# Optimization experiments

Hardware: AMD Instinct MI355X
Metric: run time of the kernel (lower is better)

Reference implementation:

```python
import jax, jax.numpy as jnp
import numpy as np

N_HEAD = 16
EPS = 1e-06


def setup_inputs() -> dict:
    key = jax.random.key(0)
    ks = jax.random.split(key, 9)
    B, S, Q, D, Dp = 16, 4096, 49, 1024, 1024
    INIT = 0.02  # GPT-2 style init scale keeps exp(scores) finite
    x = jax.random.normal(ks[0], (B, S, D), dtype=jnp.float32)
    y = jax.random.normal(ks[1], (B, Q, Dp), dtype=jnp.float32)
    # multiplicative binary mask applied to exp(scores), shaped [1,1,49,S//64,64]
    attention_mask = (jax.random.uniform(ks[2], (1, 1, Q, S // 64, 64)) > 0.5).astype(jnp.float32)
    W_attn = jax.random.normal(ks[3], (D, 2 * D), dtype=jnp.float32) * INIT
    b_attn = jnp.zeros((2 * D,), dtype=jnp.float32)
    W_mlp = jax.random.normal(ks[4], (Dp, D), dtype=jnp.float32) * INIT
    b_mlp = jnp.zeros((D,), dtype=jnp.float32)
    W_proj = jax.random.normal(ks[5], (D, Dp), dtype=jnp.float32) * INIT
    b_proj = jnp.zeros((Dp,), dtype=jnp.float32)
    return {"x": x, "y": y, "attention_mask": attention_mask,
            "W_attn": W_attn, "b_attn": b_attn, "W_mlp": W_mlp, "b_mlp": b_mlp,
            "W_proj": W_proj, "b_proj": b_proj}


def reference(x, y, attention_mask, W_attn, b_attn, W_mlp, b_mlp, W_proj, b_proj):
    B, S, D = x.shape
    Q = y.shape[1]
    H = N_HEAD
    hd = D // H
    # c_attn (Conv1D): x @ W + b -> split into key, value
    kv = x @ W_attn + b_attn                       # [B,S,2D]
    key, value = kv[..., :D], kv[..., D:]
    k = key.reshape(B, S, H, hd).transpose(0, 2, 3, 1)    # [B,H,hd,S] (k=True perm)
    v = value.reshape(B, S, H, hd).transpose(0, 2, 1, 3)  # [B,H,S,hd]
    q = (y @ W_mlp + b_mlp).reshape(B, Q, H, hd).transpose(0, 2, 1, 3)  # [B,H,Q,hd]
    # fp32 scores, scaled by sqrt(head_dim)
    w = jnp.einsum('bhqd,bhds->bhqs', q.astype(jnp.float32), k.astype(jnp.float32))
    w = w / jnp.sqrt(jnp.float32(hd))
    # custom exp + multiplicative blocked mask + epsilon-stabilized normalize
    e = (jnp.exp(w).reshape(B, H, 49, -1, 64) * attention_mask).reshape(B, H, Q, S)
    w = e / (e.sum(-1, keepdims=True) + EPS)
    # PV matmul, cast to bf16 as in the original, then merge heads
    a = jnp.einsum('bhqs,bhsd->bhqd', w, v.astype(jnp.float32)).astype(jnp.bfloat16)
    a = a.transpose(0, 2, 1, 3).reshape(B, Q, D).astype(jnp.float32)
    out = a @ W_proj + b_proj                      # c_proj
    return out
```

## Files before the change

### kernel.cpp

```cpp
#include <hip/hip_runtime.h>
#include <cstdint>

typedef __bf16 bf16x8 __attribute__((ext_vector_type(8)));
typedef float f32x4 __attribute__((ext_vector_type(4)));
typedef unsigned short u16;

#define GBAR() asm volatile("s_barrier" ::: "memory")
#define SBAR0() __builtin_amdgcn_sched_barrier(0)
#define LGKM0() do { asm volatile("s_waitcnt lgkmcnt(0)" ::: "memory"); SBAR0(); } while (0)
#define VM6()  asm volatile("s_waitcnt vmcnt(6)" ::: "memory")
#define VM8()  asm volatile("s_waitcnt vmcnt(8)" ::: "memory")
#define MFMA16(a, b, c) __builtin_amdgcn_mfma_f32_16x16x32_bf16((a), (b), (c), 0, 0, 0)

__device__ __forceinline__ u16 f2bf(float f) {
  unsigned u = __builtin_bit_cast(unsigned, f);
  u += 0x7fffu + ((u >> 16) & 1u);
  return (u16)(u >> 16);
}
__device__ __forceinline__ float bfu(ushort4 v, int r) {
  unsigned short s = (r == 0) ? v.x : (r == 1) ? v.y : (r == 2) ? v.z : v.w;
  return __builtin_bit_cast(float, (unsigned)s << 16);
}

__global__ void cast_f32_bf16(const float* __restrict__ in, u16* __restrict__ out,
                              int n4in, int n4out) {
  int i = blockIdx.x * blockDim.x + threadIdx.x;
  int stride = gridDim.x * blockDim.x;
  for (; i < n4out; i += stride) {
    ushort4 o;
    if (i < n4in) {
      float4 v = ((const float4*)in)[i];
      o.x = f2bf(v.x); o.y = f2bf(v.y); o.z = f2bf(v.z); o.w = f2bf(v.w);
    } else {
      o.x = 0; o.y = 0; o.z = 0; o.w = 0;
    }
    ((ushort4*)out)[i] = o;
  }
}

__global__ void transpose_cast(const float* __restrict__ in, u16* __restrict__ out,
                               int R, int C) {
  __shared__ float t[64][65];
  int tc = blockIdx.x * 64, tr = blockIdx.y * 64;
  int c = threadIdx.x & 63, r0 = threadIdx.x >> 6;
  #pragma unroll
  for (int p = 0; p < 16; ++p) {
    int r = p * 4 + r0;
    t[r][c] = in[(long)(tr + r) * C + (tc + c)];
  }
  __syncthreads();
  #pragma unroll
  for (int p = 0; p < 16; ++p) {
    int r = p * 4 + r0;
    out[(long)(tc + r) * R + (tr + c)] = f2bf(t[c][r]);
  }
}

__global__ void mask_prep(const float* __restrict__ in, u16* __restrict__ out) {
  __shared__ float t[64][65];
  int s0 = blockIdx.x * 64;
  int c = threadIdx.x & 63, r0 = threadIdx.x >> 6;
  #pragma unroll
  for (int p = 0; p < 16; ++p) {
    int q = p * 4 + r0;
    t[q][c] = (q < 49) ? in[(long)q * 4096 + s0 + c] : 0.f;
  }
  __syncthreads();
  #pragma unroll
  for (int p = 0; p < 16; ++p) {
    int r = p * 4 + r0;
    out[(long)(s0 + r) * 64 + c] = f2bf(t[c][r]);
  }
}

template<int MODE>
__global__ __launch_bounds__(512, 2) void gemm256(
    const u16* __restrict__ A, const u16* __restrict__ BT,
    const float* __restrict__ bias, void* __restrict__ outp)
{
  __shared__ __align__(16) char lds[131072];

  int tid = threadIdx.x;
  int l = tid & 63, w = tid >> 6;
  int wr = w >> 2, wc = w & 3;
  int lr = l & 15, lh = l >> 4;

  int bid = blockIdx.x;
  int mt, nt;
  long out_off = 0;
  const u16* Ap = A;
  const u16* BTp = BT;
  if constexpr (MODE == 0) {
    int wg = (bid & 7) * 128 + (bid >> 3);
    mt = wg >> 2; nt = wg & 3;
  } else {
    int wg = (bid & 7) * 8 + (bid >> 3);
    mt = wg & 3; nt = wg >> 2;
    int b = blockIdx.y;
    BTp = BT + (long)b * 4194304;
    out_off = (long)b * 4194304;
  }
  long Arow0 = (long)mt * 256;
  long Brow0 = (long)nt * 256;

  int rho = (w << 3) + (l >> 3);
  int csw = ((l & 7) ^ (l >> 3)) << 3;
  const u16* agA = Ap + (Arow0 + rho) * 1024 + csw;
  int browoff = (w >> 2) * 64 + (w & 3) * 8 + (l >> 3);
  const u16* agB = BTp + (Brow0 + browoff) * 1024 + csw;
  char* ldsAthr = lds + rho * 128 + (l & 7) * 16;
  char* ldsBthr = lds + 32768 + browoff * 128 + (l & 7) * 16;

  auto SA = [&](int dt, int st, int mh) {
    char* d = ldsAthr + (dt & 1) * 65536 + mh * 8192;
    const u16* s = agA + (long)st * 64 + mh * 65536;
    __builtin_amdgcn_global_load_lds(
        (const __attribute__((address_space(1))) void*)s,
        (__attribute__((address_space(3))) void*)d, 16, 0, 0);
    __builtin_amdgcn_global_load_lds(
        (const __attribute__((address_space(1))) void*)(s + 131072),
        (__attribute__((address_space(3))) void*)(d + 16384), 16, 0, 0);
  };
  auto SB = [&](int dt, int st, int h) {
    char* d = ldsBthr + (dt & 1) * 65536 + h * 4096;
    const u16* s = agB + (long)st * 64 + h * 32768;
    __builtin_amdgcn_global_load_lds(
        (const __attribute__((address_space(1))) void*)s,
        (__attribute__((address_space(3))) void*)d, 16, 0, 0);
    __builtin_amdgcn_global_load_lds(
        (const __attribute__((address_space(1))) void*)(s + 131072),
        (__attribute__((address_space(3))) void*)(d + 16384), 16, 0, 0);
  };

  int arow_b = (wr * 128 + lr) * 128;
  int brow_b = (wc * 64 + lr) * 128 + 32768;
  int xr0 = (lh ^ (lr & 7)) << 4;
  int xr1 = ((4 + lh) ^ (lr & 7)) << 4;

  f32x4 acc[8][4];
  #pragma unroll
  for (int m = 0; m < 8; ++m)
    #pragma unroll
    for (int n = 0; n < 4; ++n) acc[m][n] = f32x4{0.f, 0.f, 0.f, 0.f};

  bf16x8 af[4][2], bn0[2][2], bn1[2][2];

  auto RD_AF0 = [&](int buf) {
    #pragma unroll
    for (int m = 0; m < 4; ++m) {
      af[m][0] = *(const bf16x8*)(lds + buf + arow_b + m * 2048 + xr0);
      af[m][1] = *(const bf16x8*)(lds + buf + arow_b + m * 2048 + xr1);
    }
  };
  auto RD_AF1 = [&](int buf) {
    #pragma unroll
    for (int m = 0; m < 4; ++m) {
      af[m][0] = *(const bf16x8*)(lds + buf + arow_b + 8192 + m * 2048 + xr0);
      af[m][1] = *(const bf16x8*)(lds + buf + arow_b + 8192 + m * 2048 + xr1);
    }
  };
  auto RD_BN0 = [&](int buf) {
    #pragma unroll
    for (int n = 0; n < 2; ++n) {
      bn0[n][0] = *(const bf16x8*)(lds + buf + brow_b + n * 2048 + xr0);
      bn0[n][1] = *(const bf16x8*)(lds + buf + brow_b + n * 2048 + xr1);
    }
  };
  auto RD_BN1 = [&](int buf) {
    #pragma unroll
    for (int n = 0; n < 2; ++n) {
      bn1[n][0] = *(const bf16x8*)(lds + buf + brow_b + 4096 + n * 2048 + xr0);
      bn1[n][1] = *(const bf16x8*)(lds + buf + brow_b + 4096 + n * 2048 + xr1);
    }
  };
  auto Q = [&](int mo, int no, bf16x8 (&bn)[2][2]) {
    __builtin_amdgcn_s_setprio(1);
    #pragma unroll
    for (int m = 0; m < 4; ++m)
      #pragma unroll
      for (int n = 0; n < 2; ++n) {
        acc[mo + m][no + n] = MFMA16(af[m][0], bn[n][0], acc[mo + m][no + n]);
        acc[mo + m][no + n] = MFMA16(af[m][1], bn[n][1], acc[mo + m][no + n]);
      }
    __builtin_amdgcn_s_setprio(0);
  };

  SA(0, 0, 0); SA(0, 0, 1); SB(0, 0, 0); SB(0, 0, 1);
  SA(1, 1, 0); SA(1, 1, 1); SB(1, 1, 0);
  VM6(); GBAR();

  for (int i = 0; i < 8; ++i) {
    int t = 2 * i;
    RD_AF0(0); RD_BN0(0); SBAR0();
    SB(t + 1, t + 1, 1);
    GBAR(); LGKM0();
    Q(0, 0, bn0);
    GBAR();
    RD_BN1(0); SBAR0();
    { int tt = t + 2; SA(tt, tt < 16 ? tt : 15, 0); }
    GBAR(); LGKM0();
    Q(0, 2, bn1);
    GBAR();
    RD_AF1(0); SBAR0();
    { int tt = t + 2; SB(tt, tt < 16 ? tt : 15, 0); }
    GBAR(); LGKM0();
    Q(4, 0, bn0);
    GBAR();
    { int tt = t + 2; SA(tt, tt < 16 ? tt : 15, 1); }
    GBAR(); VM6();
    Q(4, 2, bn1);
    GBAR();
    RD_AF0(65536); RD_BN0(65536); SBAR0();
    { int tt = t + 2; SB(tt, tt < 16 ? tt : 15, 1); }
    GBAR(); LGKM0();
    Q(0, 0, bn0);
    GBAR();
    RD_BN1(65536); SBAR0();
    { int tt = t + 3; SA(tt, tt < 16 ? tt : 15, 0); }
    GBAR(); LGKM0();
    Q(0, 2, bn1);
    GBAR();
    RD_AF1(65536); SBAR0();
    { int tt = t + 3; SB(tt, tt < 16 ? tt : 15, 0); }
    GBAR(); LGKM0();
    Q(4, 0, bn0);
    GBAR();
    { int tt = t + 3; SA(tt, tt < 16 ? tt : 15, 1); }
    GBAR(); VM6();
    Q(4, 2, bn1);
    GBAR();
  }

  asm volatile("s_waitcnt vmcnt(0)" ::: "memory");

  #pragma unroll
  for (int m = 0; m < 8; ++m) {
    #pragma unroll
    for (int n = 0; n < 4; ++n) {
      #pragma unroll
      for (int r = 0; r < 4; ++r) {
        long row = Arow0 + wr * 128 + m * 16 + lh * 4 + r;
        long col = Brow0 + wc * 64 + n * 16 + lr;
        float v = acc[m][n][r];
        if constexpr (MODE == 0) {
          v += bias[col];
          long addr = (row >> 12) * 4194304 + (col >> 6) * 262144
                    + (row & 4095) * 64 + (col & 63);
          ((u16*)outp)[addr] = f2bf(v);
        } else {
          v += bias[1024 + row];
          ((u16*)outp)[out_off + row * 4096 + col] = f2bf(v);
        }
      }
    }
  }
}

template<int MODE>
__global__ __launch_bounds__(256, 2) void gemm_bt(
    const u16* __restrict__ A, const u16* __restrict__ BT,
    const float* __restrict__ bias, void* __restrict__ outp)
{
  __shared__ u16 As[128][64];
  __shared__ u16 Bs[128][64];

  int bid = blockIdx.x;
  int mt = bid >> 3, nt = bid & 7;

  int tid = threadIdx.x;
  int l = tid & 63, w = tid >> 6;
  int wr = w >> 1, wc = w & 1;
  int lr = l & 15, lh = l >> 4;

  f32x4 acc[4][4];
  #pragma unroll
  for (int i = 0; i < 4; ++i)
    #pragma unroll
    for (int j = 0; j < 4; ++j)
      acc[i][j] = f32x4{0.f, 0.f, 0.f, 0.f};

  long arow0 = (long)mt * 128;
  long brow0 = (long)nt * 128;
  int srow = w * 8 + (l >> 3);
  int scol = (l & 7) * 8;
  const u16* ag = A + (arow0 + srow) * 1024 + scol;
  const u16* bg = BT + (brow0 + srow) * 1024 + scol;
  u16* asl = &As[srow][scol];
  u16* bsl = &Bs[srow][scol];

  for (int kt = 0; kt < 16; ++kt) {
    int ko = kt * 64;
    #pragma unroll
    for (int p = 0; p < 4; ++p)
      __builtin_amdgcn_global_load_lds(
          (const __attribute__((address_space(1))) void*)(ag + (long)p * 32 * 1024 + ko),
          (__attribute__((address_space(3))) void*)(asl + p * 32 * 64), 16, 0, 0);
    #pragma unroll
    for (int p = 0; p < 4; ++p)
      __builtin_amdgcn_global_load_lds(
          (const __attribute__((address_space(1))) void*)(bg + (long)p * 32 * 1024 + ko),
          (__attribute__((address_space(3))) void*)(bsl + p * 32 * 64), 16, 0, 0);
    __syncthreads();
    #pragma unroll
    for (int kk = 0; kk < 2; ++kk) {
      bf16x8 af[4], bfr[4];
      #pragma unroll
      for (int m = 0; m < 4; ++m)
        af[m] = *(const bf16x8*)&As[wr * 64 + m * 16 + lr][kk * 32 + lh * 8];
      #pragma unroll
      for (int n = 0; n < 4; ++n)
        bfr[n] = *(const bf16x8*)&Bs[wc * 64 + n * 16 + lr][kk * 32 + lh * 8];
      #pragma unroll
      for (int m = 0; m < 4; ++m)
        #pragma unroll
        for (int n = 0; n < 4; ++n)
          acc[m][n] = MFMA16(af[m], bfr[n], acc[m][n]);
    }
    __syncthreads();
  }

  #pragma unroll
  for (int m = 0; m < 4; ++m) {
    #pragma unroll
    for (int n = 0; n < 4; ++n) {
      #pragma unroll
      for (int r = 0; r < 4; ++r) {
        int row = (int)arow0 + wr * 64 + m * 16 + lh * 4 + r;
        int col = (int)brow0 + wc * 64 + n * 16 + lr;
        float v = acc[m][n][r];
        if constexpr (MODE == 2) {
          if (row < 784) {
            v += bias[col];
            int b = row / 49, qi = row - b * 49;
            long addr = ((long)(b * 16 + (col >> 6)) * 64 + qi) * 64 + (col & 63);
            ((u16*)outp)[addr] = f2bf(v);
          }
        } else {
          if (row < 784) {
            v += bias[col];
            ((float*)outp)[(long)row * 1024 + col] = v;
          }
        }
      }
    }
  }
}

__global__ __launch_bounds__(256, 4) void attn_part(
    const u16* __restrict__ Kt, const u16* __restrict__ Vt, const u16* __restrict__ Q,
    const u16* __restrict__ maskT,
    float* __restrict__ partA, float* __restrict__ prs)
{
  __shared__ __align__(16) char lds[40960];

  int bh = blockIdx.x, chunk = blockIdx.y;
  int tid = threadIdx.x;
  int l = tid & 63, w = tid >> 6;
  int lr = l & 15, lh = l >> 4;

  const u16* Kb = Kt + (long)bh * 262144;
  const u16* Vb = Vt + (long)bh * 262144;
  const u16* Qb = Q + (long)bh * 4096;

  int t0 = chunk * 21 + (chunk > 0 ? 1 : 0);
  int nt = 21 + (chunk == 0 ? 1 : 0);
  int tmax = t0 + nt - 1;

  int strow = tid >> 3;
  int sc = tid & 7;

  auto STAGE = [&](int buf, int tt) {
    long s0 = (long)tt * 64;
    #pragma unroll
    for (int h = 0; h < 2; ++h) {
      int row = h * 32 + strow;
      int cs = (sc ^ (row & 7)) << 3;
      const u16* ksrc = Kb + (s0 + row) * 64 + cs;
      char* kdst = lds + buf * 8192 + row * 128 + sc * 16;
      __builtin_amdgcn_global_load_lds(
          (const __attribute__((address_space(1))) void*)ksrc,
          (__attribute__((address_space(3))) void*)kdst, 16, 0, 0);
      const u16* vsrc = Vb + (long)row * 4096 + s0 + cs;
      char* vdst = lds + 16384 + buf * 8192 + row * 128 + sc * 16;
      __builtin_amdgcn_global_load_lds(
          (const __attribute__((address_space(1))) void*)vsrc,
          (__attribute__((address_space(3))) void*)vdst, 16, 0, 0);
    }
  };

  bf16x8 qf[2];
  #pragma unroll
  for (int kf2 = 0; kf2 < 2; ++kf2)
    qf[kf2] = *(const bf16x8*)(Qb + (w * 16 + lr) * 64 + kf2 * 32 + lh * 8);

  bf16x8 ones;
  #pragma unroll
  for (int j = 0; j < 8; ++j) ones[j] = (__bf16)1.0f;

  f32x4 acc_a[4];
  #pragma unroll
  for (int n = 0; n < 4; ++n) acc_a[n] = f32x4{0.f, 0.f, 0.f, 0.f};
  f32x4 acc_rs = f32x4{0.f, 0.f, 0.f, 0.f};

  char* Pw = lds + 32768 + w * 2048;
  const u16* mbase = maskT + w * 16 + lh * 4;

  STAGE(0, t0);
  STAGE(1, t0 + 1);
  ushort4 mvu[4];
  #pragma unroll
  for (int sf = 0; sf < 4; ++sf)
    mvu[sf] = *(const ushort4*)(mbase + ((long)t0 * 64 + sf * 16 + lr) * 64);
  VM8();
  GBAR();

  for (int it = 0; it < nt; ++it) {
    int buf = it & 1;
    const char* Kl = lds + buf * 8192;
    const char* Vl = lds + 16384 + buf * 8192;

    int tn = it + 1 < nt ? t0 + it + 1 : tmax;
    ushort4 mvn[4];
    #pragma unroll
    for (int sf = 0; sf < 4; ++sf)
      mvn[sf] = *(const ushort4*)(mbase + ((long)tn * 64 + sf * 16 + lr) * 64);

    bf16x8 kf[4][2];
    #pragma unroll
    for (int sf = 0; sf < 4; ++sf) {
      int srw = sf * 16 + lr;
      int xb = srw & 7;
      kf[sf][0] = *(const bf16x8*)(Kl + srw * 128 + ((lh ^ xb) << 4));
      kf[sf][1] = *(const bf16x8*)(Kl + srw * 128 + (((4 + lh) ^ xb) << 4));
    }
    f32x4 lg[4];
    #pragma unroll
    for (int sf = 0; sf < 4; ++sf) {
      f32x4 t = f32x4{0.f, 0.f, 0.f, 0.f};
      t = MFMA16(qf[0], kf[sf][0], t);
      t = MFMA16(qf[1], kf[sf][1], t);
      lg[sf] = t;
    }

    bf16x8 vf[2][4];
    #pragma unroll
    for (int k2 = 0; k2 < 2; ++k2)
      #pragma unroll
      for (int n = 0; n < 4; ++n) {
        int vrow = n * 16 + lr;
        vf[k2][n] = *(const bf16x8*)(Vl + vrow * 128 + (((k2 * 4 + lh) ^ (lr & 7)) << 4));
      }

    #pragma unroll
    for (int sf = 0; sf < 4; ++sf) {
      #pragma unroll
      for (int r = 0; r < 4; ++r) {
        int qq = lh * 4 + r;
        float e = __expf(lg[sf][r] * 0.125f) * bfu(mvu[sf], r);
        int byte = (qq * 128 + (sf * 16 + lr) * 2) ^ ((qq & 7) << 4);
        *(u16*)(Pw + byte) = f2bf(e);
      }
    }

    #pragma unroll
    for (int k2 = 0; k2 < 2; ++k2) {
      int byte = (lr * 128 + k2 * 64 + lh * 16) ^ ((lr & 7) << 4);
      bf16x8 pf;
      __builtin_memcpy(&pf, Pw + byte, 16);
      #pragma unroll
      for (int n = 0; n < 4; ++n)
        acc_a[n] = MFMA16(pf, vf[k2][n], acc_a[n]);
      acc_rs = MFMA16(pf, ones, acc_rs);
    }

    LGKM0();
    GBAR();
    { int tt = it + 2 < nt ? t0 + it + 2 : tmax; STAGE(buf, tt); }
    VM8();
    GBAR();

    #pragma unroll
    for (int sf = 0; sf < 4; ++sf) mvu[sf] = mvn[sf];
  }

  long base = ((long)bh * 3 + chunk) * 64;
  #pragma unroll
  for (int r = 0; r < 4; ++r) {
    int q = w * 16 + lh * 4 + r;
    if (lr == 0) prs[base + q] = acc_rs[r];
    #pragma unroll
    for (int n = 0; n < 4; ++n)
      partA[(base + q) * 64 + n * 16 + lr] = acc_a[n][r];
  }
}

__global__ __launch_bounds__(256) void attn_reduce(
    const float* __restrict__ partA, const float* __restrict__ prs,
    u16* __restrict__ Abf)
{
  int bh = blockIdx.x;
  int t = threadIdx.x;
  int q = t >> 2, d0 = (t & 3) * 16;
  if (q >= 49) return;
  int b = bh >> 4, h = bh & 15;

  float rs = 1e-6f;
  #pragma unroll
  for (int c = 0; c < 3; ++c) rs += prs[((long)bh * 3 + c) * 64 + q];

  #pragma unroll
  for (int j = 0; j < 4; ++j) {
    float4 s = float4{0.f, 0.f, 0.f, 0.f};
    #pragma unroll
    for (int c = 0; c < 3; ++c) {
      float4 v = *(const float4*)(partA + (((long)bh * 3 + c) * 64 + q) * 64 + d0 + j * 4);
      s.x += v.x; s.y += v.y; s.z += v.z; s.w += v.w;
    }
    ushort4 o;
    o.x = f2bf(s.x / rs); o.y = f2bf(s.y / rs);
    o.z = f2bf(s.z / rs); o.w = f2bf(s.w / rs);
    *(ushort4*)(Abf + ((long)(b * 49 + q) * 1024 + h * 64 + d0 + j * 4)) = o;
  }
}

extern "C" void kernel_launch(void* const* d_in, const int* in_sizes, int n_in,
                              void* d_out, int out_size, void* d_ws, size_t ws_size,
                              hipStream_t stream) {
  const float* x      = (const float*)d_in[0];
  const float* y      = (const float*)d_in[1];
  const float* mask   = (const float*)d_in[2];
  const float* W_attn = (const float*)d_in[3];
  const float* b_attn = (const float*)d_in[4];
  const float* W_mlp  = (const float*)d_in[5];
  const float* b_mlp  = (const float*)d_in[6];
  const float* W_proj = (const float*)d_in[7];
  const float* b_proj = (const float*)d_in[8];

  if (ws_size < 417333248ULL) return;

  char* ws = (char*)d_ws;
  u16* x_bf    = (u16*)(ws);
  u16* Kt      = (u16*)(ws + 134217728L);
  u16* Vt      = (u16*)(ws + 268435456L);
  u16* WT_attn = (u16*)(ws + 402653184L);
  u16* WT_mlp  = (u16*)(ws + 406847488L);
  u16* WT_proj = (u16*)(ws + 408944640L);
  u16* y_bf    = (u16*)(ws + 411041792L);
  u16* q_ws    = (u16*)(ws + 412876800L);
  u16* a_bf    = (u16*)(ws + 414973952L);
  u16* maskT   = (u16*)(ws + 416808960L);
  float* partA = (float*)(ws);
  float* prs   = (float*)(ws + 16777216L);

  cast_f32_bf16<<<2048, 256, 0, stream>>>(x, x_bf, 16777216, 16777216);
  cast_f32_bf16<<<896, 256, 0, stream>>>(y, y_bf, 200704, 229376);
  transpose_cast<<<dim3(32, 16), 256, 0, stream>>>(W_attn, WT_attn, 1024, 2048);
  transpose_cast<<<dim3(16, 16), 256, 0, stream>>>(W_mlp, WT_mlp, 1024, 1024);
  transpose_cast<<<dim3(16, 16), 256, 0, stream>>>(W_proj, WT_proj, 1024, 1024);
  mask_prep<<<64, 256, 0, stream>>>(mask, maskT);

  gemm256<0><<<1024, 512, 0, stream>>>(x_bf, WT_attn, b_attn, Kt);
  gemm256<1><<<dim3(64, 16), 512, 0, stream>>>(WT_attn + 1048576, x_bf, b_attn, Vt);
  gemm_bt<2><<<56, 256, 0, stream>>>(y_bf, WT_mlp, b_mlp, q_ws);

  attn_part<<<dim3(256, 3), 256, 0, stream>>>(Kt, Vt, q_ws, maskT, partA, prs);
  attn_reduce<<<256, 256, 0, stream>>>(partA, prs, a_bf);

  gemm_bt<3><<<56, 256, 0, stream>>>(a_bf, WT_proj, b_proj, d_out);
}
```

Measured before the change: 493.0 us.

## Retile small GEMMs to 64x64, fuse y cast, merge transposes, split attention into 4 chunks

Replaces the 128x128 small-GEMM kernel with a 64x64 tile version using an XOR-swizzled LDS layout. The Q projection now reads fp32 y directly and converts it to bf16 while staging, which removes the separate y cast kernel. The three weight transpose launches become one launch with a z dimension, and attention is split into 4 equal chunks of 16 tiles instead of 3 uneven ones. The goal is more blocks for the small GEMMs and attention on many CUs and fewer launches, at the cost of more partial sums to reduce.

```diff
diff --git a/kernel.cpp b/kernel.cpp
--- a/kernel.cpp
+++ b/kernel.cpp
@@ -23,24 +23,28 @@
 }
 
 __global__ void cast_f32_bf16(const float* __restrict__ in, u16* __restrict__ out,
-                              int n4in, int n4out) {
+                              int n4) {
   int i = blockIdx.x * blockDim.x + threadIdx.x;
   int stride = gridDim.x * blockDim.x;
-  for (; i < n4out; i += stride) {
+  for (; i < n4; i += stride) {
+    float4 v = ((const float4*)in)[i];
     ushort4 o;
-    if (i < n4in) {
-      float4 v = ((const float4*)in)[i];
-      o.x = f2bf(v.x); o.y = f2bf(v.y); o.z = f2bf(v.z); o.w = f2bf(v.w);
-    } else {
-      o.x = 0; o.y = 0; o.z = 0; o.w = 0;
-    }
+    o.x = f2bf(v.x); o.y = f2bf(v.y); o.z = f2bf(v.z); o.w = f2bf(v.w);
     ((ushort4*)out)[i] = o;
   }
 }
 
-__global__ void transpose_cast(const float* __restrict__ in, u16* __restrict__ out,
-                               int R, int C) {
+__global__ void transpose_all(const float* __restrict__ Wa, const float* __restrict__ Wm,
+                              const float* __restrict__ Wp,
+                              u16* __restrict__ oa, u16* __restrict__ om,
+                              u16* __restrict__ op) {
   __shared__ float t[64][65];
+  int z = blockIdx.z;
+  const float* in = (z == 0) ? Wa : (z == 1) ? Wm : Wp;
+  u16* out = (z == 0) ? oa : (z == 1) ? om : op;
+  int C = (z == 0) ? 2048 : 1024;
+  const int R = 1024;
+  if (blockIdx.x * 64 >= C) return;
   int tc = blockIdx.x * 64, tr = blockIdx.y * 64;
   int c = threadIdx.x & 63, r0 = threadIdx.x >> 6;
   #pragma unroll
@@ -257,87 +261,99 @@
 }
 
 template<int MODE>
-__global__ __launch_bounds__(256, 2) void gemm_bt(
-    const u16* __restrict__ A, const u16* __restrict__ BT,
+__global__ __launch_bounds__(256, 4) void gemm64(
+    const void* __restrict__ Ap, const u16* __restrict__ BT,
     const float* __restrict__ bias, void* __restrict__ outp)
 {
-  __shared__ u16 As[128][64];
-  __shared__ u16 Bs[128][64];
+  __shared__ u16 As[64][64];
+  __shared__ u16 Bs[64][64];
 
   int bid = blockIdx.x;
-  int mt = bid >> 3, nt = bid & 7;
-
+  int mt = bid >> 4, nt = bid & 15;
   int tid = threadIdx.x;
   int l = tid & 63, w = tid >> 6;
   int wr = w >> 1, wc = w & 1;
   int lr = l & 15, lh = l >> 4;
 
-  f32x4 acc[4][4];
-  #pragma unroll
-  for (int i = 0; i < 4; ++i)
-    #pragma unroll
-    for (int j = 0; j < 4; ++j)
-      acc[i][j] = f32x4{0.f, 0.f, 0.f, 0.f};
-
-  long arow0 = (long)mt * 128;
-  long brow0 = (long)nt * 128;
-  int srow = w * 8 + (l >> 3);
-  int scol = (l & 7) * 8;
-  const u16* ag = A + (arow0 + srow) * 1024 + scol;
-  const u16* bg = BT + (brow0 + srow) * 1024 + scol;
-  u16* asl = &As[srow][scol];
-  u16* bsl = &Bs[srow][scol];
+  f32x4 acc[2][2];
+  #pragma unroll
+  for (int m = 0; m < 2; ++m)
+    #pragma unroll
+    for (int n = 0; n < 2; ++n) acc[m][n] = f32x4{0.f, 0.f, 0.f, 0.f};
+
+  long arow0 = (long)mt * 64;
+  long brow0 = (long)nt * 64;
+  int srow = tid >> 3, sc = tid & 7;
 
   for (int kt = 0; kt < 16; ++kt) {
     int ko = kt * 64;
     #pragma unroll
-    for (int p = 0; p < 4; ++p)
+    for (int p = 0; p < 2; ++p) {
+      int row = srow + p * 32;
+      int cs = (sc ^ (row & 7)) << 3;
       __builtin_amdgcn_global_load_lds(
-          (const __attribute__((address_space(1))) void*)(ag + (long)p * 32 * 1024 + ko),
-          (__attribute__((address_space(3))) void*)(asl + p * 32 * 64), 16, 0, 0);
-    #pragma unroll
-    for (int p = 0; p < 4; ++p)
-      __builtin_amdgcn_global_load_lds(
-          (const __attribute__((address_space(1))) void*)(bg + (long)p * 32 * 1024 + ko),
-          (__attribute__((address_space(3))) void*)(bsl + p * 32 * 64), 16, 0, 0);
+          (const __attribute__((address_space(1))) void*)(BT + (brow0 + row) * 1024 + ko + cs),
+          (__attribute__((address_space(3))) void*)(&Bs[row][sc * 8]), 16, 0, 0);
+      if constexpr (MODE == 3)
+        __builtin_amdgcn_global_load_lds(
+            (const __attribute__((address_space(1))) void*)((const u16*)Ap + (arow0 + row) * 1024 + ko + cs),
+            (__attribute__((address_space(3))) void*)(&As[row][sc * 8]), 16, 0, 0);
+    }
+    if constexpr (MODE == 2) {
+      #pragma unroll
+      for (int p = 0; p < 2; ++p) {
+        int row = srow + p * 32;
+        int cs = (sc ^ (row & 7)) << 3;
+        ushort4 o0 = {0, 0, 0, 0}, o1 = {0, 0, 0, 0};
+        if (arow0 + row < 784) {
+          const float* src = (const float*)Ap + (arow0 + row) * 1024 + ko + cs;
+          float4 f0 = *(const float4*)src;
+          float4 f1 = *(const float4*)(src + 4);
+          o0.x = f2bf(f0.x); o0.y = f2bf(f0.y); o0.z = f2bf(f0.z); o0.w = f2bf(f0.w);
+          o1.x = f2bf(f1.x); o1.y = f2bf(f1.y); o1.z = f2bf(f1.z); o1.w = f2bf(f1.w);
+        }
+        *(ushort4*)(&As[row][sc * 8]) = o0;
+        *(ushort4*)(&As[row][sc * 8 + 4]) = o1;
+      }
+    }
     __syncthreads();
     #pragma unroll
     for (int kk = 0; kk < 2; ++kk) {
-      bf16x8 af[4], bfr[4];
-      #pragma unroll
-      for (int m = 0; m < 4; ++m)
-        af[m] = *(const bf16x8*)&As[wr * 64 + m * 16 + lr][kk * 32 + lh * 8];
-      #pragma unroll
-      for (int n = 0; n < 4; ++n)
-        bfr[n] = *(const bf16x8*)&Bs[wc * 64 + n * 16 + lr][kk * 32 + lh * 8];
-      #pragma unroll
-      for (int m = 0; m < 4; ++m)
+      bf16x8 afr[2], bfr[2];
+      #pragma unroll
+      for (int m = 0; m < 2; ++m) {
+        int row = wr * 32 + m * 16 + lr;
+        afr[m] = *(const bf16x8*)((const char*)&As[row][0] + (((kk * 4 + lh) ^ (row & 7)) << 4));
+      }
+      #pragma unroll
+      for (int n = 0; n < 2; ++n) {
+        int row = wc * 32 + n * 16 + lr;
+        bfr[n] = *(const bf16x8*)((const char*)&Bs[row][0] + (((kk * 4 + lh) ^ (row & 7)) << 4));
+      }
+      #pragma unroll
+      for (int m = 0; m < 2; ++m)
         #pragma unroll
-        for (int n = 0; n < 4; ++n)
-          acc[m][n] = MFMA16(af[m], bfr[n], acc[m][n]);
+        for (int n = 0; n < 2; ++n)
+          acc[m][n] = MFMA16(afr[m], bfr[n], acc[m][n]);
     }
     __syncthreads();
   }
 
   #pragma unroll
-  for (int m = 0; m < 4; ++m) {
-    #pragma unroll
-    for (int n = 0; n < 4; ++n) {
+  for (int m = 0; m < 2; ++m) {
+    #pragma unroll
+    for (int n = 0; n < 2; ++n) {
       #pragma unroll
       for (int r = 0; r < 4; ++r) {
-        int row = (int)arow0 + wr * 64 + m * 16 + lh * 4 + r;
-        int col = (int)brow0 + wc * 64 + n * 16 + lr;
-        float v = acc[m][n][r];
-        if constexpr (MODE == 2) {
-          if (row < 784) {
-            v += bias[col];
+        int row = (int)arow0 + wr * 32 + m * 16 + lh * 4 + r;
+        int col = (int)brow0 + wc * 32 + n * 16 + lr;
+        if (row < 784) {
+          float v = acc[m][n][r] + bias[col];
+          if constexpr (MODE == 2) {
             int b = row / 49, qi = row - b * 49;
             long addr = ((long)(b * 16 + (col >> 6)) * 64 + qi) * 64 + (col & 63);
             ((u16*)outp)[addr] = f2bf(v);
-          }
-        } else {
-          if (row < 784) {
-            v += bias[col];
+          } else {
             ((float*)outp)[(long)row * 1024 + col] = v;
           }
         }
@@ -362,8 +378,8 @@
   const u16* Vb = Vt + (long)bh * 262144;
   const u16* Qb = Q + (long)bh * 4096;
 
-  int t0 = chunk * 21 + (chunk > 0 ? 1 : 0);
-  int nt = 21 + (chunk == 0 ? 1 : 0);
+  int t0 = chunk * 16;
+  const int nt = 16;
   int tmax = t0 + nt - 1;
 
   int strow = tid >> 3;
@@ -483,7 +499,7 @@
     for (int sf = 0; sf < 4; ++sf) mvu[sf] = mvn[sf];
   }
 
-  long base = ((long)bh * 3 + chunk) * 64;
+  long base = ((long)bh * 4 + chunk) * 64;
   #pragma unroll
   for (int r = 0; r < 4; ++r) {
     int q = w * 16 + lh * 4 + r;
@@ -506,14 +522,14 @@
 
   float rs = 1e-6f;
   #pragma unroll
-  for (int c = 0; c < 3; ++c) rs += prs[((long)bh * 3 + c) * 64 + q];
+  for (int c = 0; c < 4; ++c) rs += prs[((long)bh * 4 + c) * 64 + q];
 
   #pragma unroll
   for (int j = 0; j < 4; ++j) {
     float4 s = float4{0.f, 0.f, 0.f, 0.f};
     #pragma unroll
-    for (int c = 0; c < 3; ++c) {
-      float4 v = *(const float4*)(partA + (((long)bh * 3 + c) * 64 + q) * 64 + d0 + j * 4);
+    for (int c = 0; c < 4; ++c) {
+      float4 v = *(const float4*)(partA + (((long)bh * 4 + c) * 64 + q) * 64 + d0 + j * 4);
       s.x += v.x; s.y += v.y; s.z += v.z; s.w += v.w;
     }
     ushort4 o;
@@ -545,26 +561,23 @@
   u16* WT_attn = (u16*)(ws + 402653184L);
   u16* WT_mlp  = (u16*)(ws + 406847488L);
   u16* WT_proj = (u16*)(ws + 408944640L);
-  u16* y_bf    = (u16*)(ws + 411041792L);
   u16* q_ws    = (u16*)(ws + 412876800L);
   u16* a_bf    = (u16*)(ws + 414973952L);
   u16* maskT   = (u16*)(ws + 416808960L);
   float* partA = (float*)(ws);
   float* prs   = (float*)(ws + 16777216L);
 
-  cast_f32_bf16<<<2048, 256, 0, stream>>>(x, x_bf, 16777216, 16777216);
-  cast_f32_bf16<<<896, 256, 0, stream>>>(y, y_bf, 200704, 229376);
-  transpose_cast<<<dim3(32, 16), 256, 0, stream>>>(W_attn, WT_attn, 1024, 2048);
-  transpose_cast<<<dim3(16, 16), 256, 0, stream>>>(W_mlp, WT_mlp, 1024, 1024);
-  transpose_cast<<<dim3(16, 16), 256, 0, stream>>>(W_proj, WT_proj, 1024, 1024);
+  cast_f32_bf16<<<2048, 256, 0, stream>>>(x, x_bf, 16777216);
+  transpose_all<<<dim3(32, 16, 3), 256, 0, stream>>>(W_attn, W_mlp, W_proj,
+                                                     WT_attn, WT_mlp, WT_proj);
   mask_prep<<<64, 256, 0, stream>>>(mask, maskT);
 
   gemm256<0><<<1024, 512, 0, stream>>>(x_bf, WT_attn, b_attn, Kt);
   gemm256<1><<<dim3(64, 16), 512, 0, stream>>>(WT_attn + 1048576, x_bf, b_attn, Vt);
-  gemm_bt<2><<<56, 256, 0, stream>>>(y_bf, WT_mlp, b_mlp, q_ws);
-
-  attn_part<<<dim3(256, 3), 256, 0, stream>>>(Kt, Vt, q_ws, maskT, partA, prs);
+  gemm64<2><<<224, 256, 0, stream>>>(y, WT_mlp, b_mlp, q_ws);
+
+  attn_part<<<dim3(256, 4), 256, 0, stream>>>(Kt, Vt, q_ws, maskT, partA, prs);
   attn_reduce<<<256, 256, 0, stream>>>(partA, prs, a_bf);
 
-  gemm_bt<3><<<56, 256, 0, stream>>>(a_bf, WT_proj, b_proj, d_out);
-}
+  gemm64<3><<<224, 256, 0, stream>>>(a_bf, WT_proj, b_proj, d_out);
+}
```

After: 465.4 us. -5.6%, faster.
